# Kernel tuning notes

Measured on AMD Instinct MI355X. Metric: run time of the kernel, lower is better.

The kernel has to match this reference:

```python
import jax, jax.numpy as jnp
import numpy as np

B, R, K, S = 512, 264, 32, 9
SUB_ENDS = np.array([28, 58, 92, 121, 150, 180, 210, 240, 264], dtype=np.int32)


def setup_inputs() -> dict:
    key = jax.random.key(0)
    embeddings = jax.random.normal(key, (B, R, K), dtype=jnp.float32)
    return {"embeddings": embeddings, "subnetwork_ends": jnp.asarray(SUB_ENDS)}


def reference(embeddings, subnetwork_ends):
    # subnetwork_ends are static structural constants (cumulative block ends).
    ends = np.asarray(jax.device_get(subnetwork_ends))
    starts = np.concatenate([np.zeros(1, dtype=ends.dtype), ends[:-1]])
    sizes = ends - starts                      # [S]
    n_sub = ends.shape[0]
    seg = np.repeat(np.arange(n_sub), sizes)   # [R] segment id per ROI

    # adjacency: batched gram matrix, [B, R, R]
    adjacency = jnp.einsum('brk,bpk->brp', embeddings, embeddings)

    # intra-network adjacency: zero out cross-block entries
    intra_mask = jnp.asarray(seg[:, None] == seg[None, :])  # [R, R] bool
    intra = adjacency * intra_mask                          # [B, R, R]

    # inter-network matrix: block means via one fused segment reduce
    # (replaces the O(S^2) per-block slice+mean loop in the original)
    one_hot = jnp.asarray(np.eye(n_sub, dtype=np.float32)[seg])          # [R, S]
    counts = jnp.asarray((sizes[:, None] * sizes[None, :]).astype(np.float32))  # [S, S]
    inter = jnp.einsum('brp,rs,pt->bst', adjacency, one_hot, one_hot) / counts  # [B, S, S]

    return intra[..., None], inter[..., None], adjacency[..., None]
```

## Files before the change

kernel.cpp:

```cpp
#include <hip/hip_runtime.h>


constexpr int B_ = 512, R_ = 264, K_ = 32, S_ = 9;
constexpr long long NI_ = (long long)B_ * R_ * R_;
constexpr long long NS_ = (long long)B_ * S_ * S_;

__global__ __launch_bounds__(512) void fused_gram(
    const float* __restrict__ emb, float* __restrict__ out) {
  constexpr int ENDS[S_]   = {28, 58, 92, 121, 150, 180, 210, 240, 264};
  constexpr int STARTS[S_] = {0, 28, 58, 92, 121, 150, 180, 210, 240};

  const int b    = blockIdx.x;
  const int tid  = threadIdx.x;
  const int wave = tid >> 6;
  const int lane = tid & 63;

  __shared__ float s_inter[S_ * S_];
  if (tid < S_ * S_) s_inter[tid] = 0.0f;
  __syncthreads();

  int p, r_lo, r_hi;
  bool active;
  if (wave < 4) {
    p = wave * 64 + lane;
    r_lo = 0;
    r_hi = R_;
    active = true;
  } else {
    active = (lane < 8);
    p = 256 + (lane & 7);
    r_lo = (wave - 4) * 66;
    r_hi = r_lo + 66;
  }

  const float4* ep4 =
      reinterpret_cast<const float4*>(emb + ((size_t)b * R_ + p) * K_);
  const float4 e0 = ep4[0], e1 = ep4[1], e2 = ep4[2], e3 = ep4[3],
               e4 = ep4[4], e5 = ep4[5], e6 = ep4[6], e7 = ep4[7];

  const int sp = (p >= 28) + (p >= 58) + (p >= 92) + (p >= 121) +
                 (p >= 150) + (p >= 180) + (p >= 210) + (p >= 240);

  float* __restrict__ intra_out = out;
  float* __restrict__ inter_out = out + NI_;
  float* __restrict__ adj_out   = out + NI_ + NS_;

  const float* __restrict__ ebase = emb + (size_t)b * R_ * K_;
  const size_t brow = (size_t)b * R_ * R_ + (size_t)p;

#pragma unroll
  for (int s = 0; s < S_; ++s) {
    const int r0 = max(r_lo, STARTS[s]);
    const int r1 = min(r_hi, ENDS[s]);
    const bool diag = (sp == s);
    float racc = 0.0f;
    for (int r = r0; r < r1; ++r) {
      const float4* rr = reinterpret_cast<const float4*>(ebase + (size_t)r * K_);
      const float4 c0 = rr[0], c1 = rr[1], c2 = rr[2], c3 = rr[3],
                   c4 = rr[4], c5 = rr[5], c6 = rr[6], c7 = rr[7];
      float v0 = c0.x * e0.x + c0.y * e0.y + c0.z * e0.z + c0.w * e0.w;
      float v1 = c1.x * e1.x + c1.y * e1.y + c1.z * e1.z + c1.w * e1.w;
      float v2 = c2.x * e2.x + c2.y * e2.y + c2.z * e2.z + c2.w * e2.w;
      float v3 = c3.x * e3.x + c3.y * e3.y + c3.z * e3.z + c3.w * e3.w;
      float v4 = c4.x * e4.x + c4.y * e4.y + c4.z * e4.z + c4.w * e4.w;
      float v5 = c5.x * e5.x + c5.y * e5.y + c5.z * e5.z + c5.w * e5.w;
      float v6 = c6.x * e6.x + c6.y * e6.y + c6.z * e6.z + c6.w * e6.w;
      float v7 = c7.x * e7.x + c7.y * e7.y + c7.z * e7.z + c7.w * e7.w;
      const float v = ((v0 + v1) + (v2 + v3)) + ((v4 + v5) + (v6 + v7));

      const size_t idx = brow + (size_t)r * R_;
      if (active) {
        __builtin_nontemporal_store(v, adj_out + idx);
        __builtin_nontemporal_store(diag ? v : 0.0f, intra_out + idx);
      }
      racc += v;
    }
    if (active && r1 > r0) atomicAdd(&s_inter[s * S_ + sp], racc);
  }

  __syncthreads();
  if (tid < S_ * S_) {
    constexpr float SZ[S_] = {28.f, 30.f, 34.f, 29.f, 29.f, 30.f, 30.f, 30.f, 24.f};
    const float cnt = SZ[tid / S_] * SZ[tid % S_];
    inter_out[(size_t)b * (S_ * S_) + tid] = s_inter[tid] / cnt;
  }
}

extern "C" void kernel_launch(void* const* d_in, const int* in_sizes, int n_in,
                              void* d_out, int out_size, void* d_ws,
                              size_t ws_size, hipStream_t stream) {
  const float* emb = (const float*)d_in[0];
  float* out = (float*)d_out;
  hipLaunchKernelGGL(fused_gram, dim3(B_), dim3(512), 0, stream, emb, out);
}
```

Measured before the change: 407.1 us.

## Split into register-tiled gram kernel and algebraic segment-sum inter kernel

Replaces the per-column dot-product kernel with a 2D register-tiled gram computation. The transposed embeddings are staged in shared memory, each thread computes a 4x4 output tile, and adjacency and intra rows are written with vectorized float4 nontemporal stores. The inter matrix is moved to a separate kernel that uses the identity sum_r,p <e_r,e_p> = <sum e_r, sum e_p>, taking segment sums of embeddings and their dot products so the atomics are no longer needed. This adds a second launch, and each of the 9 stripe blocks reloads and transposes the whole embedding slice for its batch.

```diff
diff --git a/kernel.cpp b/kernel.cpp
--- a/kernel.cpp
+++ b/kernel.cpp
@@ -2,87 +2,121 @@
 
 
 constexpr int B_ = 512, R_ = 264, K_ = 32, S_ = 9;
+constexpr int RP_ = 292;
 constexpr long long NI_ = (long long)B_ * R_ * R_;
 constexpr long long NS_ = (long long)B_ * S_ * S_;
 
-__global__ __launch_bounds__(512) void fused_gram(
+typedef float vf4 __attribute__((ext_vector_type(4)));
+
+__global__ __launch_bounds__(576, 8) void adj_intra(
     const float* __restrict__ emb, float* __restrict__ out) {
-  constexpr int ENDS[S_]   = {28, 58, 92, 121, 150, 180, 210, 240, 264};
-  constexpr int STARTS[S_] = {0, 28, 58, 92, 121, 150, 180, 210, 240};
+  __shared__ float Et[K_ * RP_];
+  __shared__ unsigned char seg_lut[288];
 
-  const int b    = blockIdx.x;
-  const int tid  = threadIdx.x;
-  const int wave = tid >> 6;
-  const int lane = tid & 63;
+  const int b = blockIdx.x;
+  const int stripe = blockIdx.y;
+  const int tid = threadIdx.x;
+  const float* __restrict__ eb = emb + (size_t)b * R_ * K_;
 
-  __shared__ float s_inter[S_ * S_];
-  if (tid < S_ * S_) s_inter[tid] = 0.0f;
+  for (int idx = tid; idx < (R_ * K_) / 4; idx += 576) {
+    const int r = idx >> 3;
+    const int kq = (idx & 7) * 4;
+    const vf4 v = *reinterpret_cast<const vf4*>(eb + r * K_ + kq);
+    Et[(kq + 0) * RP_ + r] = v.x;
+    Et[(kq + 1) * RP_ + r] = v.y;
+    Et[(kq + 2) * RP_ + r] = v.z;
+    Et[(kq + 3) * RP_ + r] = v.w;
+  }
+  for (int z = tid; z < K_ * 24; z += 576) {
+    const int k = z / 24, r = 264 + z % 24;
+    Et[k * RP_ + r] = 0.0f;
+  }
+  if (tid < 288) {
+    const int x = tid;
+    seg_lut[x] = (x >= 28) + (x >= 58) + (x >= 92) + (x >= 121) +
+                 (x >= 150) + (x >= 180) + (x >= 210) + (x >= 240);
+  }
   __syncthreads();
 
-  int p, r_lo, r_hi;
-  bool active;
-  if (wave < 4) {
-    p = wave * 64 + lane;
-    r_lo = 0;
-    r_hi = R_;
-    active = true;
-  } else {
-    active = (lane < 8);
-    p = 256 + (lane & 7);
-    r_lo = (wave - 4) * 66;
-    r_hi = r_lo + 66;
+  const int wave = tid >> 6, lane = tid & 63;
+  const int lx = lane & 7, ly = lane >> 3;
+  const int i0 = stripe * 32 + ly * 4;
+  const int j0 = wave * 32 + lx * 4;
+
+  vf4 acc0 = {0, 0, 0, 0}, acc1 = {0, 0, 0, 0};
+  vf4 acc2 = {0, 0, 0, 0}, acc3 = {0, 0, 0, 0};
+#pragma unroll 4
+  for (int k = 0; k < K_; ++k) {
+    const vf4 av = *reinterpret_cast<const vf4*>(Et + k * RP_ + i0);
+    const vf4 bv = *reinterpret_cast<const vf4*>(Et + k * RP_ + j0);
+    acc0 += av.x * bv;
+    acc1 += av.y * bv;
+    acc2 += av.z * bv;
+    acc3 += av.w * bv;
   }
 
-  const float4* ep4 =
-      reinterpret_cast<const float4*>(emb + ((size_t)b * R_ + p) * K_);
-  const float4 e0 = ep4[0], e1 = ep4[1], e2 = ep4[2], e3 = ep4[3],
-               e4 = ep4[4], e5 = ep4[5], e6 = ep4[6], e7 = ep4[7];
+  if (j0 < R_) {
+    float* __restrict__ intra_out = out;
+    float* __restrict__ adj_out = out + NI_ + NS_;
+    const int sj0 = seg_lut[j0], sj1 = seg_lut[j0 + 1];
+    const int sj2 = seg_lut[j0 + 2], sj3 = seg_lut[j0 + 3];
+    const size_t base = (size_t)b * R_ * R_ + (size_t)j0;
+    const vf4 accs[4] = {acc0, acc1, acc2, acc3};
+#pragma unroll
+    for (int ii = 0; ii < 4; ++ii) {
+      const int i = i0 + ii;
+      if (i < R_) {
+        const vf4 v = accs[ii];
+        const int si = seg_lut[i];
+        vf4 m;
+        m.x = (si == sj0) ? v.x : 0.0f;
+        m.y = (si == sj1) ? v.y : 0.0f;
+        m.z = (si == sj2) ? v.z : 0.0f;
+        m.w = (si == sj3) ? v.w : 0.0f;
+        const size_t idx = base + (size_t)i * R_;
+        __builtin_nontemporal_store(v, reinterpret_cast<vf4*>(adj_out + idx));
+        __builtin_nontemporal_store(m, reinterpret_cast<vf4*>(intra_out + idx));
+      }
+    }
+  }
+}
 
-  const int sp = (p >= 28) + (p >= 58) + (p >= 92) + (p >= 121) +
-                 (p >= 150) + (p >= 180) + (p >= 210) + (p >= 240);
+__global__ __launch_bounds__(256) void inter_k(
+    const float* __restrict__ emb, float* __restrict__ out) {
+  constexpr int ENDS[S_] = {28, 58, 92, 121, 150, 180, 210, 240, 264};
+  constexpr int STARTS[S_] = {0, 28, 58, 92, 121, 150, 180, 210, 240};
+  constexpr float SZ[S_] = {28.f, 30.f, 34.f, 29.f, 29.f, 30.f, 30.f, 30.f, 24.f};
 
-  float* __restrict__ intra_out = out;
-  float* __restrict__ inter_out = out + NI_;
-  float* __restrict__ adj_out   = out + NI_ + NS_;
+  __shared__ float ps[S_ * 8 * 32];
+  __shared__ float ss[32 * 12];
 
-  const float* __restrict__ ebase = emb + (size_t)b * R_ * K_;
-  const size_t brow = (size_t)b * R_ * R_ + (size_t)p;
+  const int b = blockIdx.x, tid = threadIdx.x;
+  const int k = tid & 31, q = tid >> 5;
+  const float* __restrict__ eb = emb + (size_t)b * R_ * K_;
 
 #pragma unroll
   for (int s = 0; s < S_; ++s) {
-    const int r0 = max(r_lo, STARTS[s]);
-    const int r1 = min(r_hi, ENDS[s]);
-    const bool diag = (sp == s);
-    float racc = 0.0f;
-    for (int r = r0; r < r1; ++r) {
-      const float4* rr = reinterpret_cast<const float4*>(ebase + (size_t)r * K_);
-      const float4 c0 = rr[0], c1 = rr[1], c2 = rr[2], c3 = rr[3],
-                   c4 = rr[4], c5 = rr[5], c6 = rr[6], c7 = rr[7];
-      float v0 = c0.x * e0.x + c0.y * e0.y + c0.z * e0.z + c0.w * e0.w;
-      float v1 = c1.x * e1.x + c1.y * e1.y + c1.z * e1.z + c1.w * e1.w;
-      float v2 = c2.x * e2.x + c2.y * e2.y + c2.z * e2.z + c2.w * e2.w;
-      float v3 = c3.x * e3.x + c3.y * e3.y + c3.z * e3.z + c3.w * e3.w;
-      float v4 = c4.x * e4.x + c4.y * e4.y + c4.z * e4.z + c4.w * e4.w;
-      float v5 = c5.x * e5.x + c5.y * e5.y + c5.z * e5.z + c5.w * e5.w;
-      float v6 = c6.x * e6.x + c6.y * e6.y + c6.z * e6.z + c6.w * e6.w;
-      float v7 = c7.x * e7.x + c7.y * e7.y + c7.z * e7.z + c7.w * e7.w;
-      const float v = ((v0 + v1) + (v2 + v3)) + ((v4 + v5) + (v6 + v7));
-
-      const size_t idx = brow + (size_t)r * R_;
-      if (active) {
-        __builtin_nontemporal_store(v, adj_out + idx);
-        __builtin_nontemporal_store(diag ? v : 0.0f, intra_out + idx);
-      }
-      racc += v;
-    }
-    if (active && r1 > r0) atomicAdd(&s_inter[s * S_ + sp], racc);
+    const int lo = STARTS[s], len = ENDS[s] - STARTS[s];
+    const int c0 = lo + (len * q) / 8, c1 = lo + (len * (q + 1)) / 8;
+    float a = 0.0f;
+    for (int r = c0; r < c1; ++r) a += eb[r * K_ + k];
+    ps[(s * 8 + q) * 32 + k] = a;
   }
-
+  __syncthreads();
+  for (int c = tid; c < S_ * 32; c += 256) {
+    const int s = c >> 5, kk = c & 31;
+    float a = 0.0f;
+#pragma unroll
+    for (int qq = 0; qq < 8; ++qq) a += ps[(s * 8 + qq) * 32 + kk];
+    ss[kk * 12 + s] = a;
+  }
   __syncthreads();
   if (tid < S_ * S_) {
-    constexpr float SZ[S_] = {28.f, 30.f, 34.f, 29.f, 29.f, 30.f, 30.f, 30.f, 24.f};
-    const float cnt = SZ[tid / S_] * SZ[tid % S_];
-    inter_out[(size_t)b * (S_ * S_) + tid] = s_inter[tid] / cnt;
+    const int s = tid / S_, t = tid % S_;
+    float d = 0.0f;
+    for (int kk = 0; kk < 32; ++kk) d += ss[kk * 12 + s] * ss[kk * 12 + t];
+    d /= (SZ[s] * SZ[t]);
+    __builtin_nontemporal_store(d, out + NI_ + (size_t)b * (S_ * S_) + tid);
   }
 }
 
@@ -91,5 +125,6 @@
                               size_t ws_size, hipStream_t stream) {
   const float* emb = (const float*)d_in[0];
   float* out = (float*)d_out;
-  hipLaunchKernelGGL(fused_gram, dim3(B_), dim3(512), 0, stream, emb, out);
+  hipLaunchKernelGGL(adj_intra, dim3(B_, 9), dim3(576), 0, stream, emb, out);
+  hipLaunchKernelGGL(inter_k, dim3(B_), dim3(256), 0, stream, emb, out);
 }
```

Result: faster. 389.3 us (-4.4%).
